# Optimization experiments

Hardware: AMD Instinct MI355X
Metric: run time of the kernel (lower is better)

The kernel has to match this reference:

```python
import jax, jax.numpy as jnp
import numpy as np

B, Q, K, H, DV = 16, 256, 256, 256, 256


def setup_inputs() -> dict:
    key = jax.random.key(0)
    ks = jax.random.split(key, 6)
    return {
        "queries": jax.random.normal(ks[0], (B, Q, H), dtype=jnp.float32),
        "keys": jax.random.normal(ks[1], (B, K, H), dtype=jnp.float32),
        "values": jax.random.normal(ks[2], (B, K, DV), dtype=jnp.float32),
        "W_q": jax.random.normal(ks[3], (H, H), dtype=jnp.float32) / np.sqrt(H),
        "W_k": jax.random.normal(ks[4], (H, H), dtype=jnp.float32) / np.sqrt(H),
        "w_v": jax.random.normal(ks[5], (H,), dtype=jnp.float32) / np.sqrt(H),
    }


def reference(queries, keys, values, W_q, W_k, w_v):
    # Linear projections (nn.Linear: x @ W.T), bias-free
    q = jnp.einsum("bqd,hd->bqh", queries, W_q)  # [B,Q,H]
    k = jnp.einsum("bkd,hd->bkh", keys, W_k)      # [B,K,H]
    # Broadcast add -> tanh -> scalar projection
    features = jnp.tanh(q[:, :, None, :] + k[:, None, :, :])  # [B,Q,K,H]
    scores = jnp.einsum("bqkh,h->bqk", features, w_v)          # [B,Q,K]
    attn = jax.nn.softmax(scores, axis=-1)                      # [B,Q,K]
    return jnp.einsum("bqk,bkv->bqv", attn, values)            # [B,Q,DV]
```

## Files before the change

### kernel.cpp

```cpp
#include <hip/hip_runtime.h>
#include <hip/hip_fp16.h>

#define Bn 16
#define Qn 256
#define Kn 256
#define Hn 256
#define DVn 256

constexpr float C2    = 2.8853900817779268f;
constexpr float LOG2E = 1.4426950408889634f;

typedef __attribute__((ext_vector_type(8))) short   bf16x8;
typedef __attribute__((ext_vector_type(8))) _Float16 halfx8;
typedef __attribute__((ext_vector_type(4))) float   f32x4;

__device__ __forceinline__ float fast_exp2(float x) { return __builtin_amdgcn_exp2f(x); }
__device__ __forceinline__ float fast_rcp(float x)  { return __builtin_amdgcn_rcpf(x); }

__device__ __forceinline__ unsigned short f2bf(float x) {
    unsigned u = __float_as_uint(x);
    u += 0x7fffu + ((u >> 16) & 1u);
    return (unsigned short)(u >> 16);
}

__global__ __launch_bounds__(256)
void prep_kernel(const float* __restrict__ q, const float* __restrict__ kx,
                 const float* __restrict__ wq, const float* __restrict__ wk,
                 const float* __restrict__ V,
                 unsigned short* __restrict__ Xb, unsigned short* __restrict__ Wb,
                 _Float16* __restrict__ Vt)
{
    __shared__ _Float16 T[64][72];
    const int tid = threadIdx.x;
    const int bx  = blockIdx.x;
    if (bx < 1024) {
        const int g = bx * 256 + tid;
        {
            const float* xs = (g < 131072) ? (q + (size_t)g * 8)
                                           : (kx + (size_t)(g - 131072) * 8);
            float4 x0 = *(const float4*)xs;
            float4 x1 = *(const float4*)(xs + 4);
            ushort4 o0, o1;
            o0.x = f2bf(x0.x); o0.y = f2bf(x0.y); o0.z = f2bf(x0.z); o0.w = f2bf(x0.w);
            o1.x = f2bf(x1.x); o1.y = f2bf(x1.y); o1.z = f2bf(x1.z); o1.w = f2bf(x1.w);
            *(ushort4*)(Xb + (size_t)g * 8)     = o0;
            *(ushort4*)(Xb + (size_t)g * 8 + 4) = o1;
        }
        if (g < 32768) {
            const float* ws = (g < 16384) ? (wq + (size_t)g * 4)
                                          : (wk + (size_t)(g - 16384) * 4);
            float4 w0 = *(const float4*)ws;
            ushort4 o;
            o.x = f2bf(w0.x); o.y = f2bf(w0.y); o.z = f2bf(w0.z); o.w = f2bf(w0.w);
            *(ushort4*)(Wb + (size_t)g * 4) = o;
        }
        return;
    }
    const int tb  = bx - 1024;
    const int b   = tb >> 4;
    const int t2  = tb & 15;
    const int kt  = t2 >> 2, dvt = t2 & 3;
    {
        const int kk = tid >> 2, c4 = (tid & 3) * 16;
        const float* src = V + ((size_t)(b * Kn + kt * 64 + kk)) * DVn + dvt * 64 + c4;
        #pragma unroll
        for (int j4 = 0; j4 < 4; ++j4) {
            float4 v = *(const float4*)(src + j4 * 4);
            T[c4 + j4*4 + 0][kk] = (_Float16)v.x;
            T[c4 + j4*4 + 1][kk] = (_Float16)v.y;
            T[c4 + j4*4 + 2][kk] = (_Float16)v.z;
            T[c4 + j4*4 + 3][kk] = (_Float16)v.w;
        }
    }
    __syncthreads();
    {
        const int d = tid >> 2, kc = (tid & 3) * 16;
        const uint4* srcl = (const uint4*)&T[d][kc];
        uint4* dst = (uint4*)(Vt + (size_t)b * (DVn * Kn) + (size_t)(dvt * 64 + d) * Kn + kt * 64 + kc);
        dst[0] = srcl[0];
        dst[1] = srcl[1];
    }
}

__global__ __launch_bounds__(256)
void proj_mfma_kernel(const unsigned short* __restrict__ Xb,
                      const unsigned short* __restrict__ Wb,
                      float* __restrict__ Eq, unsigned short* __restrict__ Ekb)
{
    const int tid  = threadIdx.x;
    const int wvid = tid >> 6, lane = tid & 63;
    const int m0   = blockIdx.x * 16;
    const int n0   = wvid * 64;
    const bool isQ = (m0 < 4096);
    const int r16  = lane & 15, q8 = (lane >> 4) * 8;

    const unsigned short* Xrow  = Xb + (size_t)(m0 + r16) * 256 + q8;
    const unsigned short* Wbase = Wb + (isQ ? 0 : 65536);

    bf16x8 afr[8];
    #pragma unroll
    for (int s = 0; s < 8; ++s) afr[s] = *(const bf16x8*)(Xrow + s * 32);

    f32x4 acc[4];
    #pragma unroll
    for (int nt = 0; nt < 4; ++nt) {
        const unsigned short* Wrow = Wbase + (size_t)(n0 + nt * 16 + r16) * 256 + q8;
        f32x4 c = {0.f, 0.f, 0.f, 0.f};
        #pragma unroll
        for (int s = 0; s < 8; ++s) {
            bf16x8 bfr = *(const bf16x8*)(Wrow + s * 32);
            c = __builtin_amdgcn_mfma_f32_16x16x32_bf16(afr[s], bfr, c, 0, 0, 0);
        }
        acc[nt] = c;
    }
    const int rbase = (lane >> 4) * 4;
    #pragma unroll
    for (int nt = 0; nt < 4; ++nt) {
        const int n = n0 + nt * 16 + r16;
        #pragma unroll
        for (int r = 0; r < 4; ++r) {
            const int m = m0 + rbase + r;
            const float val = fast_exp2(C2 * acc[nt][r]);
            if (isQ) {
                Eq[(size_t)m * 256 + n] = val;
            } else {
                const int kr = m - 4096, b = kr >> 8, kk = kr & 255;
                Ekb[(((size_t)(b * 64 + (n >> 2))) * 256 + kk) * 4 + (n & 3)] = f2bf(val);
            }
        }
    }
}

__global__ __launch_bounds__(256)
void scores_kernel(const float* __restrict__ Eq, const unsigned short* __restrict__ Ekb,
                   const float* __restrict__ wv, _Float16* __restrict__ P)
{
    const int b  = blockIdx.y;
    const int q0 = blockIdx.x * 4;
    __shared__ float sredM[4][4];
    __shared__ float sredS[4][4];
    const int tid = threadIdx.x;

    const float* eq0 = Eq + (size_t)(b * Qn + q0) * Hn;

    float sc[4] = {0.f, 0.f, 0.f, 0.f};
    const uint2* ekp = (const uint2*)Ekb + (size_t)b * 16384 + tid;
    uint2 e[4];
    #pragma unroll
    for (int g = 0; g < 4; ++g) e[g] = ekp[g * 256];
    for (int it = 0; it < 16; ++it) {
        uint2 en[4];
        if (it < 15) {
            #pragma unroll
            for (int g = 0; g < 4; ++g) en[g] = ekp[(4 * (it + 1) + g) * 256];
        }
        const int h0 = it * 16;
        float ek[16];
        #pragma unroll
        for (int g = 0; g < 4; ++g) {
            ek[4*g+0] = __uint_as_float(e[g].x << 16);
            ek[4*g+1] = __uint_as_float(e[g].x & 0xFFFF0000u);
            ek[4*g+2] = __uint_as_float(e[g].y << 16);
            ek[4*g+3] = __uint_as_float(e[g].y & 0xFFFF0000u);
        }
        #pragma unroll
        for (int g = 0; g < 4; ++g) {
            const float4 wa = *(const float4*)(wv + h0 + 4 * g);
            #pragma unroll
            for (int qq = 0; qq < 4; ++qq) {
                const float4 ea = *(const float4*)(eq0 + qq * 256 + h0 + 4 * g);
                float a = sc[qq];
                a = fmaf(wa.x, fast_rcp(fmaf(ea.x, ek[4*g+0], 1.f)), a);
                a = fmaf(wa.y, fast_rcp(fmaf(ea.y, ek[4*g+1], 1.f)), a);
                a = fmaf(wa.z, fast_rcp(fmaf(ea.z, ek[4*g+2], 1.f)), a);
                a = fmaf(wa.w, fast_rcp(fmaf(ea.w, ek[4*g+3], 1.f)), a);
                sc[qq] = a;
            }
        }
        #pragma unroll
        for (int g = 0; g < 4; ++g) e[g] = en[g];
    }

    const int w = tid >> 6, lane = tid & 63;
    #pragma unroll
    for (int qq = 0; qq < 4; ++qq) {
        sc[qq] = -2.0f * sc[qq];
        float mx = sc[qq];
        #pragma unroll
        for (int off = 32; off; off >>= 1) mx = fmaxf(mx, __shfl_xor(mx, off, 64));
        if (lane == 0) sredM[qq][w] = mx;
    }
    __syncthreads();
    float pq[4];
    #pragma unroll
    for (int qq = 0; qq < 4; ++qq) {
        const float mx = fmaxf(fmaxf(sredM[qq][0], sredM[qq][1]),
                               fmaxf(sredM[qq][2], sredM[qq][3]));
        pq[qq] = fast_exp2(LOG2E * (sc[qq] - mx));
        float s = pq[qq];
        #pragma unroll
        for (int off = 32; off; off >>= 1) s += __shfl_xor(s, off, 64);
        if (lane == 0) sredS[qq][w] = s;
    }
    __syncthreads();
    #pragma unroll
    for (int qq = 0; qq < 4; ++qq) {
        const float rinv = fast_rcp(sredS[qq][0] + sredS[qq][1] + sredS[qq][2] + sredS[qq][3]);
        P[(size_t)(b * Qn + q0 + qq) * Kn + tid] = (_Float16)(pq[qq] * rinv);
    }
}

__global__ __launch_bounds__(256)
void pv_mfma_kernel(const _Float16* __restrict__ P, const _Float16* __restrict__ Vt,
                    float* __restrict__ out)
{
    const int tid  = threadIdx.x;
    const int wvid = tid >> 6, lane = tid & 63;
    const int bx   = blockIdx.x;
    const int b    = bx >> 5;
    const int t2   = bx & 31;
    const int q0   = (t2 >> 1) * 16;
    const int nb   = (t2 & 1) * 128 + wvid * 32;
    const int r16  = lane & 15, q8 = (lane >> 4) * 8;

    const _Float16* Prow = P + (size_t)b * (Qn * Kn) + (size_t)(q0 + r16) * Kn + q8;
    halfx8 afr[8];
    #pragma unroll
    for (int s = 0; s < 8; ++s) afr[s] = *(const halfx8*)(Prow + s * 32);

    f32x4 acc[2];
    #pragma unroll
    for (int nt = 0; nt < 2; ++nt) {
        const _Float16* Vrow = Vt + (size_t)b * (DVn * Kn) + (size_t)(nb + nt * 16 + r16) * Kn + q8;
        f32x4 c = {0.f, 0.f, 0.f, 0.f};
        #pragma unroll
        for (int s = 0; s < 8; ++s) {
            halfx8 bfr = *(const halfx8*)(Vrow + s * 32);
            c = __builtin_amdgcn_mfma_f32_16x16x32_f16(afr[s], bfr, c, 0, 0, 0);
        }
        acc[nt] = c;
    }
    const int rbase = (lane >> 4) * 4;
    #pragma unroll
    for (int nt = 0; nt < 2; ++nt) {
        const int n = nb + nt * 16 + r16;
        #pragma unroll
        for (int r = 0; r < 4; ++r) {
            out[(size_t)(b * Qn + q0 + rbase + r) * DVn + n] = acc[nt][r];
        }
    }
}

extern "C" void kernel_launch(void* const* d_in, const int* in_sizes, int n_in,
                              void* d_out, int out_size, void* d_ws, size_t ws_size,
                              hipStream_t stream) {
    const float* queries = (const float*)d_in[0];
    const float* keys    = (const float*)d_in[1];
    const float* values  = (const float*)d_in[2];
    const float* W_q     = (const float*)d_in[3];
    const float* W_k     = (const float*)d_in[4];
    const float* w_v     = (const float*)d_in[5];
    float* out = (float*)d_out;

    char* wsb = (char*)d_ws;
    float*          Eq  = (float*)(wsb);
    unsigned short* Ekb = (unsigned short*)(wsb + (4u << 20));
    unsigned short* Xb  = (unsigned short*)(wsb + (6u << 20));
    unsigned short* Wb  = (unsigned short*)(wsb + (10u << 20));
    _Float16*       Vt  = (_Float16*)(wsb + (10u << 20) + (256u << 10));
    _Float16*       P   = (_Float16*)(wsb + (12u << 20) + (256u << 10));

    prep_kernel<<<dim3(1280), 256, 0, stream>>>(queries, keys, W_q, W_k, values,
                                                Xb, Wb, Vt);
    proj_mfma_kernel<<<dim3(512), 256, 0, stream>>>(Xb, Wb, Eq, Ekb);
    scores_kernel<<<dim3(64, 16), 256, 0, stream>>>(Eq, Ekb, w_v, P);
    pv_mfma_kernel<<<dim3(512), 256, 0, stream>>>(P, Vt, out);
}
```

Measured before the change: 130.3 us.

## Fuse four kernels into one cooperative kernel with grid-wide syncs

Merges the prep, projection, scores and PV kernels into one cooperative launch of 512 blocks, with grid.sync() and threadfences between phases. The goal is to remove the launch gaps and per-kernel tail effects of four separate launches. The cost is fixed work distribution: prep and scores now loop twice per block. Occupancy is tied to cooperative residency limits, and grid barriers have their own overhead.

```diff
diff --git a/kernel.cpp b/kernel.cpp
--- a/kernel.cpp
+++ b/kernel.cpp
@@ -1,5 +1,8 @@
 #include <hip/hip_runtime.h>
 #include <hip/hip_fp16.h>
+#include <hip/hip_cooperative_groups.h>
+
+namespace cg = cooperative_groups;
 
 #define Bn 16
 #define Qn 256
@@ -10,9 +13,9 @@
 constexpr float C2    = 2.8853900817779268f;
 constexpr float LOG2E = 1.4426950408889634f;
 
-typedef __attribute__((ext_vector_type(8))) short   bf16x8;
+typedef __attribute__((ext_vector_type(8))) short    bf16x8;
 typedef __attribute__((ext_vector_type(8))) _Float16 halfx8;
-typedef __attribute__((ext_vector_type(4))) float   f32x4;
+typedef __attribute__((ext_vector_type(4))) float    f32x4;
 
 __device__ __forceinline__ float fast_exp2(float x) { return __builtin_amdgcn_exp2f(x); }
 __device__ __forceinline__ float fast_rcp(float x)  { return __builtin_amdgcn_rcpf(x); }
@@ -23,230 +26,228 @@
     return (unsigned short)(u >> 16);
 }
 
-__global__ __launch_bounds__(256)
-void prep_kernel(const float* __restrict__ q, const float* __restrict__ kx,
+__global__ __launch_bounds__(256, 2)
+void mega_kernel(const float* __restrict__ q, const float* __restrict__ kx,
                  const float* __restrict__ wq, const float* __restrict__ wk,
-                 const float* __restrict__ V,
+                 const float* __restrict__ V, const float* __restrict__ wv,
+                 float* __restrict__ out,
+                 float* __restrict__ Eq, unsigned short* __restrict__ Ekb,
                  unsigned short* __restrict__ Xb, unsigned short* __restrict__ Wb,
-                 _Float16* __restrict__ Vt)
+                 _Float16* __restrict__ Vt, _Float16* __restrict__ P)
 {
+    cg::grid_group grid = cg::this_grid();
     __shared__ _Float16 T[64][72];
-    const int tid = threadIdx.x;
-    const int bx  = blockIdx.x;
-    if (bx < 1024) {
-        const int g = bx * 256 + tid;
-        {
-            const float* xs = (g < 131072) ? (q + (size_t)g * 8)
-                                           : (kx + (size_t)(g - 131072) * 8);
-            float4 x0 = *(const float4*)xs;
-            float4 x1 = *(const float4*)(xs + 4);
-            ushort4 o0, o1;
-            o0.x = f2bf(x0.x); o0.y = f2bf(x0.y); o0.z = f2bf(x0.z); o0.w = f2bf(x0.w);
-            o1.x = f2bf(x1.x); o1.y = f2bf(x1.y); o1.z = f2bf(x1.z); o1.w = f2bf(x1.w);
-            *(ushort4*)(Xb + (size_t)g * 8)     = o0;
-            *(ushort4*)(Xb + (size_t)g * 8 + 4) = o1;
-        }
-        if (g < 32768) {
-            const float* ws = (g < 16384) ? (wq + (size_t)g * 4)
-                                          : (wk + (size_t)(g - 16384) * 4);
-            float4 w0 = *(const float4*)ws;
-            ushort4 o;
-            o.x = f2bf(w0.x); o.y = f2bf(w0.y); o.z = f2bf(w0.z); o.w = f2bf(w0.w);
-            *(ushort4*)(Wb + (size_t)g * 4) = o;
-        }
-        return;
-    }
-    const int tb  = bx - 1024;
-    const int b   = tb >> 4;
-    const int t2  = tb & 15;
-    const int kt  = t2 >> 2, dvt = t2 & 3;
-    {
-        const int kk = tid >> 2, c4 = (tid & 3) * 16;
-        const float* src = V + ((size_t)(b * Kn + kt * 64 + kk)) * DVn + dvt * 64 + c4;
-        #pragma unroll
-        for (int j4 = 0; j4 < 4; ++j4) {
-            float4 v = *(const float4*)(src + j4 * 4);
-            T[c4 + j4*4 + 0][kk] = (_Float16)v.x;
-            T[c4 + j4*4 + 1][kk] = (_Float16)v.y;
-            T[c4 + j4*4 + 2][kk] = (_Float16)v.z;
-            T[c4 + j4*4 + 3][kk] = (_Float16)v.w;
-        }
-    }
-    __syncthreads();
-    {
-        const int d = tid >> 2, kc = (tid & 3) * 16;
-        const uint4* srcl = (const uint4*)&T[d][kc];
-        uint4* dst = (uint4*)(Vt + (size_t)b * (DVn * Kn) + (size_t)(dvt * 64 + d) * Kn + kt * 64 + kc);
-        dst[0] = srcl[0];
-        dst[1] = srcl[1];
-    }
-}
-
-__global__ __launch_bounds__(256)
-void proj_mfma_kernel(const unsigned short* __restrict__ Xb,
-                      const unsigned short* __restrict__ Wb,
-                      float* __restrict__ Eq, unsigned short* __restrict__ Ekb)
-{
-    const int tid  = threadIdx.x;
-    const int wvid = tid >> 6, lane = tid & 63;
-    const int m0   = blockIdx.x * 16;
-    const int n0   = wvid * 64;
-    const bool isQ = (m0 < 4096);
-    const int r16  = lane & 15, q8 = (lane >> 4) * 8;
-
-    const unsigned short* Xrow  = Xb + (size_t)(m0 + r16) * 256 + q8;
-    const unsigned short* Wbase = Wb + (isQ ? 0 : 65536);
-
-    bf16x8 afr[8];
-    #pragma unroll
-    for (int s = 0; s < 8; ++s) afr[s] = *(const bf16x8*)(Xrow + s * 32);
-
-    f32x4 acc[4];
-    #pragma unroll
-    for (int nt = 0; nt < 4; ++nt) {
-        const unsigned short* Wrow = Wbase + (size_t)(n0 + nt * 16 + r16) * 256 + q8;
-        f32x4 c = {0.f, 0.f, 0.f, 0.f};
-        #pragma unroll
-        for (int s = 0; s < 8; ++s) {
-            bf16x8 bfr = *(const bf16x8*)(Wrow + s * 32);
-            c = __builtin_amdgcn_mfma_f32_16x16x32_bf16(afr[s], bfr, c, 0, 0, 0);
-        }
-        acc[nt] = c;
-    }
-    const int rbase = (lane >> 4) * 4;
-    #pragma unroll
-    for (int nt = 0; nt < 4; ++nt) {
-        const int n = n0 + nt * 16 + r16;
-        #pragma unroll
-        for (int r = 0; r < 4; ++r) {
-            const int m = m0 + rbase + r;
-            const float val = fast_exp2(C2 * acc[nt][r]);
-            if (isQ) {
-                Eq[(size_t)m * 256 + n] = val;
-            } else {
-                const int kr = m - 4096, b = kr >> 8, kk = kr & 255;
-                Ekb[(((size_t)(b * 64 + (n >> 2))) * 256 + kk) * 4 + (n & 3)] = f2bf(val);
-            }
-        }
-    }
-}
-
-__global__ __launch_bounds__(256)
-void scores_kernel(const float* __restrict__ Eq, const unsigned short* __restrict__ Ekb,
-                   const float* __restrict__ wv, _Float16* __restrict__ P)
-{
-    const int b  = blockIdx.y;
-    const int q0 = blockIdx.x * 4;
     __shared__ float sredM[4][4];
     __shared__ float sredS[4][4];
     const int tid = threadIdx.x;
-
-    const float* eq0 = Eq + (size_t)(b * Qn + q0) * Hn;
-
-    float sc[4] = {0.f, 0.f, 0.f, 0.f};
-    const uint2* ekp = (const uint2*)Ekb + (size_t)b * 16384 + tid;
-    uint2 e[4];
+    const int bx  = blockIdx.x;
+
     #pragma unroll
-    for (int g = 0; g < 4; ++g) e[g] = ekp[g * 256];
-    for (int it = 0; it < 16; ++it) {
-        uint2 en[4];
-        if (it < 15) {
-            #pragma unroll
-            for (int g = 0; g < 4; ++g) en[g] = ekp[(4 * (it + 1) + g) * 256];
-        }
-        const int h0 = it * 16;
-        float ek[16];
-        #pragma unroll
-        for (int g = 0; g < 4; ++g) {
-            ek[4*g+0] = __uint_as_float(e[g].x << 16);
-            ek[4*g+1] = __uint_as_float(e[g].x & 0xFFFF0000u);
-            ek[4*g+2] = __uint_as_float(e[g].y << 16);
-            ek[4*g+3] = __uint_as_float(e[g].y & 0xFFFF0000u);
-        }
-        #pragma unroll
-        for (int g = 0; g < 4; ++g) {
-            const float4 wa = *(const float4*)(wv + h0 + 4 * g);
-            #pragma unroll
-            for (int qq = 0; qq < 4; ++qq) {
-                const float4 ea = *(const float4*)(eq0 + qq * 256 + h0 + 4 * g);
-                float a = sc[qq];
-                a = fmaf(wa.x, fast_rcp(fmaf(ea.x, ek[4*g+0], 1.f)), a);
-                a = fmaf(wa.y, fast_rcp(fmaf(ea.y, ek[4*g+1], 1.f)), a);
-                a = fmaf(wa.z, fast_rcp(fmaf(ea.z, ek[4*g+2], 1.f)), a);
-                a = fmaf(wa.w, fast_rcp(fmaf(ea.w, ek[4*g+3], 1.f)), a);
-                sc[qq] = a;
-            }
-        }
-        #pragma unroll
-        for (int g = 0; g < 4; ++g) e[g] = en[g];
-    }
-
-    const int w = tid >> 6, lane = tid & 63;
-    #pragma unroll
-    for (int qq = 0; qq < 4; ++qq) {
-        sc[qq] = -2.0f * sc[qq];
-        float mx = sc[qq];
-        #pragma unroll
-        for (int off = 32; off; off >>= 1) mx = fmaxf(mx, __shfl_xor(mx, off, 64));
-        if (lane == 0) sredM[qq][w] = mx;
-    }
-    __syncthreads();
-    float pq[4];
-    #pragma unroll
-    for (int qq = 0; qq < 4; ++qq) {
-        const float mx = fmaxf(fmaxf(sredM[qq][0], sredM[qq][1]),
-                               fmaxf(sredM[qq][2], sredM[qq][3]));
-        pq[qq] = fast_exp2(LOG2E * (sc[qq] - mx));
-        float s = pq[qq];
-        #pragma unroll
-        for (int off = 32; off; off >>= 1) s += __shfl_xor(s, off, 64);
-        if (lane == 0) sredS[qq][w] = s;
-    }
-    __syncthreads();
-    #pragma unroll
-    for (int qq = 0; qq < 4; ++qq) {
-        const float rinv = fast_rcp(sredS[qq][0] + sredS[qq][1] + sredS[qq][2] + sredS[qq][3]);
-        P[(size_t)(b * Qn + q0 + qq) * Kn + tid] = (_Float16)(pq[qq] * rinv);
-    }
-}
-
-__global__ __launch_bounds__(256)
-void pv_mfma_kernel(const _Float16* __restrict__ P, const _Float16* __restrict__ Vt,
-                    float* __restrict__ out)
-{
-    const int tid  = threadIdx.x;
-    const int wvid = tid >> 6, lane = tid & 63;
-    const int bx   = blockIdx.x;
-    const int b    = bx >> 5;
-    const int t2   = bx & 31;
-    const int q0   = (t2 >> 1) * 16;
-    const int nb   = (t2 & 1) * 128 + wvid * 32;
-    const int r16  = lane & 15, q8 = (lane >> 4) * 8;
-
-    const _Float16* Prow = P + (size_t)b * (Qn * Kn) + (size_t)(q0 + r16) * Kn + q8;
-    halfx8 afr[8];
-    #pragma unroll
-    for (int s = 0; s < 8; ++s) afr[s] = *(const halfx8*)(Prow + s * 32);
-
-    f32x4 acc[2];
-    #pragma unroll
-    for (int nt = 0; nt < 2; ++nt) {
-        const _Float16* Vrow = Vt + (size_t)b * (DVn * Kn) + (size_t)(nb + nt * 16 + r16) * Kn + q8;
-        f32x4 c = {0.f, 0.f, 0.f, 0.f};
-        #pragma unroll
-        for (int s = 0; s < 8; ++s) {
-            halfx8 bfr = *(const halfx8*)(Vrow + s * 32);
-            c = __builtin_amdgcn_mfma_f32_16x16x32_f16(afr[s], bfr, c, 0, 0, 0);
-        }
-        acc[nt] = c;
-    }
-    const int rbase = (lane >> 4) * 4;
-    #pragma unroll
-    for (int nt = 0; nt < 2; ++nt) {
-        const int n = nb + nt * 16 + r16;
-        #pragma unroll
-        for (int r = 0; r < 4; ++r) {
-            out[(size_t)(b * Qn + q0 + rbase + r) * DVn + n] = acc[nt][r];
+    for (int r = 0; r < 2; ++r) {
+        const int g = (bx * 2 + r) * 256 + tid;
+        const float* xs = (g < 131072) ? (q + (size_t)g * 8)
+                                       : (kx + (size_t)(g - 131072) * 8);
+        float4 x0 = *(const float4*)xs;
+        float4 x1 = *(const float4*)(xs + 4);
+        ushort4 o0, o1;
+        o0.x = f2bf(x0.x); o0.y = f2bf(x0.y); o0.z = f2bf(x0.z); o0.w = f2bf(x0.w);
+        o1.x = f2bf(x1.x); o1.y = f2bf(x1.y); o1.z = f2bf(x1.z); o1.w = f2bf(x1.w);
+        *(ushort4*)(Xb + (size_t)g * 8)     = o0;
+        *(ushort4*)(Xb + (size_t)g * 8 + 4) = o1;
+    }
+    if (bx < 128) {
+        const int g = bx * 256 + tid;
+        const float* ws = (g < 16384) ? (wq + (size_t)g * 4)
+                                      : (wk + (size_t)(g - 16384) * 4);
+        float4 w0 = *(const float4*)ws;
+        ushort4 o;
+        o.x = f2bf(w0.x); o.y = f2bf(w0.y); o.z = f2bf(w0.z); o.w = f2bf(w0.w);
+        *(ushort4*)(Wb + (size_t)g * 4) = o;
+    }
+    if (bx >= 128 && bx < 384) {
+        const int tb  = bx - 128;
+        const int b   = tb >> 4;
+        const int t2  = tb & 15;
+        const int kt  = t2 >> 2, dvt = t2 & 3;
+        {
+            const int kk = tid >> 2, c4 = (tid & 3) * 16;
+            const float* src = V + ((size_t)(b * Kn + kt * 64 + kk)) * DVn + dvt * 64 + c4;
+            #pragma unroll
+            for (int j4 = 0; j4 < 4; ++j4) {
+                float4 v = *(const float4*)(src + j4 * 4);
+                T[c4 + j4*4 + 0][kk] = (_Float16)v.x;
+                T[c4 + j4*4 + 1][kk] = (_Float16)v.y;
+                T[c4 + j4*4 + 2][kk] = (_Float16)v.z;
+                T[c4 + j4*4 + 3][kk] = (_Float16)v.w;
+            }
+        }
+        __syncthreads();
+        {
+            const int d = tid >> 2, kc = (tid & 3) * 16;
+            const uint4* srcl = (const uint4*)&T[d][kc];
+            uint4* dst = (uint4*)(Vt + (size_t)b * (DVn * Kn) + (size_t)(dvt * 64 + d) * Kn + kt * 64 + kc);
+            dst[0] = srcl[0];
+            dst[1] = srcl[1];
+        }
+    }
+    __threadfence();
+    grid.sync();
+
+    {
+        const int wvid = tid >> 6, lane = tid & 63;
+        const int m0   = bx * 16;
+        const int n0   = wvid * 64;
+        const bool isQ = (m0 < 4096);
+        const int r16  = lane & 15, q8 = (lane >> 4) * 8;
+
+        const unsigned short* Xrow  = Xb + (size_t)(m0 + r16) * 256 + q8;
+        const unsigned short* Wbase = Wb + (isQ ? 0 : 65536);
+
+        bf16x8 afr[8];
+        #pragma unroll
+        for (int s = 0; s < 8; ++s) afr[s] = *(const bf16x8*)(Xrow + s * 32);
+
+        f32x4 acc[4];
+        #pragma unroll
+        for (int nt = 0; nt < 4; ++nt) {
+            const unsigned short* Wrow = Wbase + (size_t)(n0 + nt * 16 + r16) * 256 + q8;
+            f32x4 c = {0.f, 0.f, 0.f, 0.f};
+            #pragma unroll
+            for (int s = 0; s < 8; ++s) {
+                bf16x8 bfr = *(const bf16x8*)(Wrow + s * 32);
+                c = __builtin_amdgcn_mfma_f32_16x16x32_bf16(afr[s], bfr, c, 0, 0, 0);
+            }
+            acc[nt] = c;
+        }
+        const int rbase = (lane >> 4) * 4;
+        #pragma unroll
+        for (int nt = 0; nt < 4; ++nt) {
+            const int n = n0 + nt * 16 + r16;
+            #pragma unroll
+            for (int r = 0; r < 4; ++r) {
+                const int m = m0 + rbase + r;
+                const float val = fast_exp2(C2 * acc[nt][r]);
+                if (isQ) {
+                    Eq[(size_t)m * 256 + n] = val;
+                } else {
+                    const int kr = m - 4096, b = kr >> 8, kk = kr & 255;
+                    Ekb[(((size_t)(b * 64 + (n >> 2))) * 256 + kk) * 4 + (n & 3)] = f2bf(val);
+                }
+            }
+        }
+    }
+    __threadfence();
+    grid.sync();
+
+    for (int rr = 0; rr < 2; ++rr) {
+        const int u  = bx + 512 * rr;
+        const int b  = u >> 6;
+        const int q0 = (u & 63) * 4;
+        const float* eq0 = Eq + (size_t)(b * Qn + q0) * Hn;
+
+        float sc[4] = {0.f, 0.f, 0.f, 0.f};
+        const uint2* ekp = (const uint2*)Ekb + (size_t)b * 16384 + tid;
+        uint2 e[4];
+        #pragma unroll
+        for (int g = 0; g < 4; ++g) e[g] = ekp[g * 256];
+        for (int it = 0; it < 16; ++it) {
+            uint2 en[4];
+            if (it < 15) {
+                #pragma unroll
+                for (int g = 0; g < 4; ++g) en[g] = ekp[(4 * (it + 1) + g) * 256];
+            }
+            const int h0 = it * 16;
+            float ek[16];
+            #pragma unroll
+            for (int g = 0; g < 4; ++g) {
+                ek[4*g+0] = __uint_as_float(e[g].x << 16);
+                ek[4*g+1] = __uint_as_float(e[g].x & 0xFFFF0000u);
+                ek[4*g+2] = __uint_as_float(e[g].y << 16);
+                ek[4*g+3] = __uint_as_float(e[g].y & 0xFFFF0000u);
+            }
+            #pragma unroll
+            for (int g = 0; g < 4; ++g) {
+                const float4 wa = *(const float4*)(wv + h0 + 4 * g);
+                #pragma unroll
+                for (int qq = 0; qq < 4; ++qq) {
+                    const float4 ea = *(const float4*)(eq0 + qq * 256 + h0 + 4 * g);
+                    float a = sc[qq];
+                    a = fmaf(wa.x, fast_rcp(fmaf(ea.x, ek[4*g+0], 1.f)), a);
+                    a = fmaf(wa.y, fast_rcp(fmaf(ea.y, ek[4*g+1], 1.f)), a);
+                    a = fmaf(wa.z, fast_rcp(fmaf(ea.z, ek[4*g+2], 1.f)), a);
+                    a = fmaf(wa.w, fast_rcp(fmaf(ea.w, ek[4*g+3], 1.f)), a);
+                    sc[qq] = a;
+                }
+            }
+            #pragma unroll
+            for (int g = 0; g < 4; ++g) e[g] = en[g];
+        }
+
+        const int w = tid >> 6, lane = tid & 63;
+        #pragma unroll
+        for (int qq = 0; qq < 4; ++qq) {
+            sc[qq] = -2.0f * sc[qq];
+            float mx = sc[qq];
+            #pragma unroll
+            for (int off = 32; off; off >>= 1) mx = fmaxf(mx, __shfl_xor(mx, off, 64));
+            if (lane == 0) sredM[qq][w] = mx;
+        }
+        __syncthreads();
+        float pq[4];
+        #pragma unroll
+        for (int qq = 0; qq < 4; ++qq) {
+            const float mx = fmaxf(fmaxf(sredM[qq][0], sredM[qq][1]),
+                                   fmaxf(sredM[qq][2], sredM[qq][3]));
+            pq[qq] = fast_exp2(LOG2E * (sc[qq] - mx));
+            float s = pq[qq];
+            #pragma unroll
+            for (int off = 32; off; off >>= 1) s += __shfl_xor(s, off, 64);
+            if (lane == 0) sredS[qq][w] = s;
+        }
+        __syncthreads();
+        #pragma unroll
+        for (int qq = 0; qq < 4; ++qq) {
+            const float rinv = fast_rcp(sredS[qq][0] + sredS[qq][1] + sredS[qq][2] + sredS[qq][3]);
+            P[(size_t)(b * Qn + q0 + qq) * Kn + tid] = (_Float16)(pq[qq] * rinv);
+        }
+        __syncthreads();
+    }
+    __threadfence();
+    grid.sync();
+
+    {
+        const int wvid = tid >> 6, lane = tid & 63;
+        const int b    = bx >> 5;
+        const int t2   = bx & 31;
+        const int q0   = (t2 >> 1) * 16;
+        const int nb   = (t2 & 1) * 128 + wvid * 32;
+        const int r16  = lane & 15, q8 = (lane >> 4) * 8;
+
+        const _Float16* Prow = P + (size_t)b * (Qn * Kn) + (size_t)(q0 + r16) * Kn + q8;
+        halfx8 afr[8];
+        #pragma unroll
+        for (int s = 0; s < 8; ++s) afr[s] = *(const halfx8*)(Prow + s * 32);
+
+        f32x4 acc[2];
+        #pragma unroll
+        for (int nt = 0; nt < 2; ++nt) {
+            const _Float16* Vrow = Vt + (size_t)b * (DVn * Kn) + (size_t)(nb + nt * 16 + r16) * Kn + q8;
+            f32x4 c = {0.f, 0.f, 0.f, 0.f};
+            #pragma unroll
+            for (int s = 0; s < 8; ++s) {
+                halfx8 bfr = *(const halfx8*)(Vrow + s * 32);
+                c = __builtin_amdgcn_mfma_f32_16x16x32_f16(afr[s], bfr, c, 0, 0, 0);
+            }
+            acc[nt] = c;
+        }
+        const int rbase = (lane >> 4) * 4;
+        #pragma unroll
+        for (int nt = 0; nt < 2; ++nt) {
+            const int n = nb + nt * 16 + r16;
+            #pragma unroll
+            for (int r = 0; r < 4; ++r) {
+                out[(size_t)(b * Qn + q0 + rbase + r) * DVn + n] = acc[nt][r];
+            }
         }
     }
 }
@@ -270,9 +271,11 @@
     _Float16*       Vt  = (_Float16*)(wsb + (10u << 20) + (256u << 10));
     _Float16*       P   = (_Float16*)(wsb + (12u << 20) + (256u << 10));
 
-    prep_kernel<<<dim3(1280), 256, 0, stream>>>(queries, keys, W_q, W_k, values,
-                                                Xb, Wb, Vt);
-    proj_mfma_kernel<<<dim3(512), 256, 0, stream>>>(Xb, Wb, Eq, Ekb);
-    scores_kernel<<<dim3(64, 16), 256, 0, stream>>>(Eq, Ekb, w_v, P);
-    pv_mfma_kernel<<<dim3(512), 256, 0, stream>>>(P, Vt, out);
+    void* args[] = {
+        (void*)&queries, (void*)&keys, (void*)&W_q, (void*)&W_k,
+        (void*)&values, (void*)&w_v, (void*)&out,
+        (void*)&Eq, (void*)&Ekb, (void*)&Xb, (void*)&Wb, (void*)&Vt, (void*)&P
+    };
+    hipLaunchCooperativeKernel((const void*)mega_kernel, dim3(512), dim3(256),
+                               args, 0, stream);
 }
```

Result: slower. 462.6 us (+255.1%).

## Split scores kernel into two query rows per block with two keys per thread

Applied to the files above, without the earlier changes.

The scores kernel now handles 2 query rows per block instead of 4. Each half of the block owns one query row, and each thread computes two keys (k and k+128). Accumulation is split across two interleaved partial sums per key to shorten the FMA dependency chains, and the query row index is made wave-uniform with readfirstlane so its loads can be scalar. The grid doubles to 2048 blocks. The trade-off is that each block re-reads the key features for only 2 queries rather than 4, which doubles that traffic.

```diff
diff --git a/kernel.cpp b/kernel.cpp
--- a/kernel.cpp
+++ b/kernel.cpp
@@ -10,9 +10,9 @@
 constexpr float C2    = 2.8853900817779268f;
 constexpr float LOG2E = 1.4426950408889634f;
 
-typedef __attribute__((ext_vector_type(8))) short   bf16x8;
+typedef __attribute__((ext_vector_type(8))) short    bf16x8;
 typedef __attribute__((ext_vector_type(8))) _Float16 halfx8;
-typedef __attribute__((ext_vector_type(4))) float   f32x4;
+typedef __attribute__((ext_vector_type(4))) float    f32x4;
 
 __device__ __forceinline__ float fast_exp2(float x) { return __builtin_amdgcn_exp2f(x); }
 __device__ __forceinline__ float fast_rcp(float x)  { return __builtin_amdgcn_rcpf(x); }
@@ -135,79 +135,81 @@
 void scores_kernel(const float* __restrict__ Eq, const unsigned short* __restrict__ Ekb,
                    const float* __restrict__ wv, _Float16* __restrict__ P)
 {
-    const int b  = blockIdx.y;
-    const int q0 = blockIdx.x * 4;
-    __shared__ float sredM[4][4];
-    __shared__ float sredS[4][4];
+    const int b   = blockIdx.y;
+    const int q0  = blockIdx.x * 2;
     const int tid = threadIdx.x;
-
-    const float* eq0 = Eq + (size_t)(b * Qn + q0) * Hn;
-
-    float sc[4] = {0.f, 0.f, 0.f, 0.f};
-    const uint2* ekp = (const uint2*)Ekb + (size_t)b * 16384 + tid;
-    uint2 e[4];
-    #pragma unroll
-    for (int g = 0; g < 4; ++g) e[g] = ekp[g * 256];
+    const int half = tid >> 7;
+    const int kl   = tid & 127;
+    __shared__ float sredM[2][2];
+    __shared__ float sredS[2][2];
+
+    const int qrow = __builtin_amdgcn_readfirstlane(b * Qn + q0 + half);
+    const float* eq0 = Eq + (size_t)qrow * Hn;
+
+    float4 acc = {0.f, 0.f, 0.f, 0.f};
+    const uint2* ekp = (const uint2*)Ekb + (size_t)b * 16384 + kl;
+    uint2 e0[4], e1[4];
+    #pragma unroll
+    for (int g = 0; g < 4; ++g) { e0[g] = ekp[g * 256]; e1[g] = ekp[g * 256 + 128]; }
     for (int it = 0; it < 16; ++it) {
-        uint2 en[4];
+        uint2 en0[4], en1[4];
         if (it < 15) {
             #pragma unroll
-            for (int g = 0; g < 4; ++g) en[g] = ekp[(4 * (it + 1) + g) * 256];
+            for (int g = 0; g < 4; ++g) {
+                en0[g] = ekp[(4 * (it + 1) + g) * 256];
+                en1[g] = ekp[(4 * (it + 1) + g) * 256 + 128];
+            }
         }
         const int h0 = it * 16;
-        float ek[16];
         #pragma unroll
         for (int g = 0; g < 4; ++g) {
-            ek[4*g+0] = __uint_as_float(e[g].x << 16);
-            ek[4*g+1] = __uint_as_float(e[g].x & 0xFFFF0000u);
-            ek[4*g+2] = __uint_as_float(e[g].y << 16);
-            ek[4*g+3] = __uint_as_float(e[g].y & 0xFFFF0000u);
-        }
-        #pragma unroll
-        for (int g = 0; g < 4; ++g) {
+            const float ka0 = __uint_as_float(e0[g].x << 16);
+            const float ka1 = __uint_as_float(e0[g].x & 0xFFFF0000u);
+            const float ka2 = __uint_as_float(e0[g].y << 16);
+            const float ka3 = __uint_as_float(e0[g].y & 0xFFFF0000u);
+            const float kb0 = __uint_as_float(e1[g].x << 16);
+            const float kb1 = __uint_as_float(e1[g].x & 0xFFFF0000u);
+            const float kb2 = __uint_as_float(e1[g].y << 16);
+            const float kb3 = __uint_as_float(e1[g].y & 0xFFFF0000u);
             const float4 wa = *(const float4*)(wv + h0 + 4 * g);
-            #pragma unroll
-            for (int qq = 0; qq < 4; ++qq) {
-                const float4 ea = *(const float4*)(eq0 + qq * 256 + h0 + 4 * g);
-                float a = sc[qq];
-                a = fmaf(wa.x, fast_rcp(fmaf(ea.x, ek[4*g+0], 1.f)), a);
-                a = fmaf(wa.y, fast_rcp(fmaf(ea.y, ek[4*g+1], 1.f)), a);
-                a = fmaf(wa.z, fast_rcp(fmaf(ea.z, ek[4*g+2], 1.f)), a);
-                a = fmaf(wa.w, fast_rcp(fmaf(ea.w, ek[4*g+3], 1.f)), a);
-                sc[qq] = a;
-            }
-        }
-        #pragma unroll
-        for (int g = 0; g < 4; ++g) e[g] = en[g];
-    }
-
-    const int w = tid >> 6, lane = tid & 63;
-    #pragma unroll
-    for (int qq = 0; qq < 4; ++qq) {
-        sc[qq] = -2.0f * sc[qq];
-        float mx = sc[qq];
-        #pragma unroll
-        for (int off = 32; off; off >>= 1) mx = fmaxf(mx, __shfl_xor(mx, off, 64));
-        if (lane == 0) sredM[qq][w] = mx;
-    }
+            const float4 ea = *(const float4*)(eq0 + h0 + 4 * g);
+            const int c = g & 1;
+            float a0 = (c == 0) ? acc.x : acc.y;
+            float a1 = (c == 0) ? acc.z : acc.w;
+            a0 = fmaf(wa.x, fast_rcp(fmaf(ea.x, ka0, 1.f)), a0);
+            a1 = fmaf(wa.x, fast_rcp(fmaf(ea.x, kb0, 1.f)), a1);
+            a0 = fmaf(wa.y, fast_rcp(fmaf(ea.y, ka1, 1.f)), a0);
+            a1 = fmaf(wa.y, fast_rcp(fmaf(ea.y, kb1, 1.f)), a1);
+            a0 = fmaf(wa.z, fast_rcp(fmaf(ea.z, ka2, 1.f)), a0);
+            a1 = fmaf(wa.z, fast_rcp(fmaf(ea.z, kb2, 1.f)), a1);
+            a0 = fmaf(wa.w, fast_rcp(fmaf(ea.w, ka3, 1.f)), a0);
+            a1 = fmaf(wa.w, fast_rcp(fmaf(ea.w, kb3, 1.f)), a1);
+            if (c == 0) { acc.x = a0; acc.z = a1; } else { acc.y = a0; acc.w = a1; }
+        }
+        #pragma unroll
+        for (int g = 0; g < 4; ++g) { e0[g] = en0[g]; e1[g] = en1[g]; }
+    }
+
+    const int winh = (tid >> 6) & 1;
+    const int lane = tid & 63;
+    float s0 = -2.0f * (acc.x + acc.y);
+    float s1 = -2.0f * (acc.z + acc.w);
+    float mx = fmaxf(s0, s1);
+    #pragma unroll
+    for (int off = 32; off; off >>= 1) mx = fmaxf(mx, __shfl_xor(mx, off, 64));
+    if (lane == 0) sredM[half][winh] = mx;
     __syncthreads();
-    float pq[4];
-    #pragma unroll
-    for (int qq = 0; qq < 4; ++qq) {
-        const float mx = fmaxf(fmaxf(sredM[qq][0], sredM[qq][1]),
-                               fmaxf(sredM[qq][2], sredM[qq][3]));
-        pq[qq] = fast_exp2(LOG2E * (sc[qq] - mx));
-        float s = pq[qq];
-        #pragma unroll
-        for (int off = 32; off; off >>= 1) s += __shfl_xor(s, off, 64);
-        if (lane == 0) sredS[qq][w] = s;
-    }
+    mx = fmaxf(sredM[half][0], sredM[half][1]);
+    const float p0 = fast_exp2(LOG2E * (s0 - mx));
+    const float p1 = fast_exp2(LOG2E * (s1 - mx));
+    float s = p0 + p1;
+    #pragma unroll
+    for (int off = 32; off; off >>= 1) s += __shfl_xor(s, off, 64);
+    if (lane == 0) sredS[half][winh] = s;
     __syncthreads();
-    #pragma unroll
-    for (int qq = 0; qq < 4; ++qq) {
-        const float rinv = fast_rcp(sredS[qq][0] + sredS[qq][1] + sredS[qq][2] + sredS[qq][3]);
-        P[(size_t)(b * Qn + q0 + qq) * Kn + tid] = (_Float16)(pq[qq] * rinv);
-    }
+    const float rinv = fast_rcp(sredS[half][0] + sredS[half][1]);
+    P[(size_t)qrow * Kn + kl]       = (_Float16)(p0 * rinv);
+    P[(size_t)qrow * Kn + kl + 128] = (_Float16)(p1 * rinv);
 }
 
 __global__ __launch_bounds__(256)
@@ -273,6 +275,6 @@
     prep_kernel<<<dim3(1280), 256, 0, stream>>>(queries, keys, W_q, W_k, values,
                                                 Xb, Wb, Vt);
     proj_mfma_kernel<<<dim3(512), 256, 0, stream>>>(Xb, Wb, Eq, Ekb);
-    scores_kernel<<<dim3(64, 16), 256, 0, stream>>>(Eq, Ekb, w_v, P);
+    scores_kernel<<<dim3(128, 16), 256, 0, stream>>>(Eq, Ekb, w_v, P);
     pv_mfma_kernel<<<dim3(512), 256, 0, stream>>>(P, Vt, out);
 }
```

Result: slower. 134.2 us (+3.0%).
